# Optimization experiments

Measured on AMD Instinct MI355X. Metric: run time of the kernel, lower is better.

The kernel has to match this reference:

```python
import jax, jax.numpy as jnp
import numpy as np
import math

B, N0, DEG = 32, 1584, 4
E = B * N0 * DEG
FIN, HID, EDIM, ROUTE, HEADS = 32, 64, 8, 16, 4
NEG = 0.2  # leaky_relu negative slope (alpha)
K1 = math.ceil(0.8 * N0)   # 1268 nodes/graph after pool1
K2 = math.ceil(0.8 * K1)   # 1015 after pool2
K3 = math.ceil(0.8 * K2)   # 812 after pool3


def _gatv2(x, src, dst, emask, edge_attr, Wl, bl, Wr, br, We, att, bo, num_nodes):
    # PyG GATv2Conv, concat=False (mean over heads), edge_dim, eval mode (no dropout)
    xl = (x @ Wl + bl).reshape(-1, HEADS, HID)            # source transform  [N,H,C]
    xr = (x @ Wr + br).reshape(-1, HEADS, HID)            # target transform  [N,H,C]
    ee = (edge_attr @ We).reshape(-1, HEADS, HID)         # edge transform    [E,H,C]
    m = jax.nn.leaky_relu(xl[src] + xr[dst] + ee, NEG)    # [E,H,C]
    logits = jnp.einsum('ehc,hc->eh', m, att)             # [E,H]
    logits = jnp.where(emask[:, None], logits, -jnp.inf)
    mx = jax.ops.segment_max(logits, dst, num_segments=num_nodes)
    mx = jnp.where(jnp.isfinite(mx), mx, 0.0)             # nodes w/o in-edges
    ex = jnp.where(emask[:, None], jnp.exp(logits - mx[dst]), 0.0)
    den = jax.ops.segment_sum(ex, dst, num_segments=num_nodes)
    alpha = ex / jnp.maximum(den[dst], 1e-16)             # segment softmax over dst
    out = jax.ops.segment_sum(alpha[:, :, None] * xl[src], dst, num_segments=num_nodes)
    return out.mean(axis=1) + bo                          # concat=False -> head mean


def _topk(x, src, dst, emask, w, n_per, k):
    # PyG TopKPooling(ratio=0.8): score = tanh(x.w/||w||); keep top-k per graph,
    # scale kept features by score; keep edges whose endpoints both survive.
    s = jnp.tanh((x @ w) / jnp.linalg.norm(w))            # [B*n_per]
    _, idx = jax.lax.top_k(s.reshape(B, n_per), k)        # [B,k]
    perm = (idx + jnp.arange(B)[:, None] * n_per).reshape(-1)
    x_new = x[perm] * s[perm][:, None]
    new_id = jnp.full((B * n_per,), -1, jnp.int32).at[perm].set(
        jnp.arange(B * k, dtype=jnp.int32))
    nsrc, ndst = new_id[src], new_id[dst]
    m = emask & (nsrc >= 0) & (ndst >= 0)
    return x_new, jnp.where(m, nsrc, 0), jnp.where(m, ndst, 0), m


def _readout(x, k):
    # global mean pool || global max pool (nodes are grouped per graph, k each)
    xb = x.reshape(B, k, HID)
    return jnp.concatenate([xb.mean(1), xb.max(1)], axis=1)


def _forward(x, edge_attr, edge_index,
             g1_Wl, g1_bl, g1_Wr, g1_br, g1_We, g1_att, g1_b,
             g2_Wl, g2_bl, g2_Wr, g2_br, g2_We, g2_att, g2_b,
             g3_Wl, g3_bl, g3_Wr, g3_br, g3_We, g3_att, g3_b,
             p1_w, p2_w, p3_w,
             fc1_W, fc1_b, fc2_W, fc2_b, fc3_W, fc3_b):
    src, dst = edge_index[0], edge_index[1]
    emask = jnp.ones((E,), bool)
    h = jax.nn.relu(_gatv2(x, src, dst, emask, edge_attr,
                           g1_Wl, g1_bl, g1_Wr, g1_br, g1_We, g1_att, g1_b, B * N0))
    h, src, dst, emask = _topk(h, src, dst, emask, p1_w, N0, K1)
    x1 = _readout(h, K1)
    h = jax.nn.relu(_gatv2(h, src, dst, emask, edge_attr,
                           g2_Wl, g2_bl, g2_Wr, g2_br, g2_We, g2_att, g2_b, B * K1))
    h, src, dst, emask = _topk(h, src, dst, emask, p2_w, K1, K2)
    x2 = _readout(h, K2)
    h = jax.nn.relu(_gatv2(h, src, dst, emask, edge_attr,
                           g3_Wl, g3_bl, g3_Wr, g3_br, g3_We, g3_att, g3_b, B * K2))
    h, src, dst, emask = _topk(h, src, dst, emask, p3_w, K2, K3)
    x3 = _readout(h, K3)
    r = x1 + x2 + x3                                      # [B, 2*HID]
    h = jax.nn.relu(r @ fc1_W + fc1_b)
    h = jax.nn.relu(h @ fc2_W + fc2_b)                    # dropout results unused in source
    return jax.nn.softmax(h @ fc3_W + fc3_b, axis=1)      # [B, ROUTE]


def setup_inputs() -> dict:
    key = jax.random.key(0)
    ks = iter(jax.random.split(key, 64))
    def nrm(shape, scale):
        return jax.random.normal(next(ks), shape, jnp.float32) * scale
    x = nrm((B * N0, FIN), 1.0)
    srcl = jax.random.randint(next(ks), (B, N0 * DEG), 0, N0)
    dstl = jax.random.randint(next(ks), (B, N0 * DEG), 0, N0)
    off = (jnp.arange(B) * N0)[:, None]
    edge_index = jnp.stack([(srcl + off).reshape(-1),
                            (dstl + off).reshape(-1)]).astype(jnp.int32)
    edge_attr = nrm((E, EDIM), 1.0)
    batch = jnp.repeat(jnp.arange(B, dtype=jnp.int32), N0)
    inp = {"x": x, "edge_attr": edge_attr, "edge_index": edge_index, "batch": batch}
    for li, fin in ((1, FIN), (2, HID), (3, HID)):
        g = 1.0 / np.sqrt(fin)
        inp[f"g{li}_Wl"] = nrm((fin, HEADS * HID), g)
        inp[f"g{li}_bl"] = nrm((HEADS * HID,), 0.02)
        inp[f"g{li}_Wr"] = nrm((fin, HEADS * HID), g)
        inp[f"g{li}_br"] = nrm((HEADS * HID,), 0.02)
        inp[f"g{li}_We"] = nrm((EDIM, HEADS * HID), 1.0 / np.sqrt(EDIM))
        inp[f"g{li}_att"] = nrm((HEADS, HID), 1.0 / np.sqrt(HID))
        inp[f"g{li}_b"] = nrm((HID,), 0.02)
    for li in (1, 2, 3):
        inp[f"p{li}_w"] = nrm((HID,), 1.0 / np.sqrt(HID))
    for fin, fout, nm in ((2 * HID, HID, "fc1"), (HID, HID, "fc2"), (HID, ROUTE, "fc3")):
        inp[f"{nm}_W"] = nrm((fin, fout), 1.0 / np.sqrt(fin))
        inp[f"{nm}_b"] = nrm((fout,), 0.02)
    return inp


def reference(x, edge_attr, edge_index, batch,
              g1_Wl, g1_bl, g1_Wr, g1_br, g1_We, g1_att, g1_b,
              g2_Wl, g2_bl, g2_Wr, g2_br, g2_We, g2_att, g2_b,
              g3_Wl, g3_bl, g3_Wr, g3_br, g3_We, g3_att, g3_b,
              p1_w, p2_w, p3_w,
              fc1_W, fc1_b, fc2_W, fc2_b, fc3_W, fc3_b):
    # batch is implicit: nodes are laid out grouped per graph with static sizes
    del batch
    return _forward(x, edge_attr, edge_index,
                    g1_Wl, g1_bl, g1_Wr, g1_br, g1_We, g1_att, g1_b,
                    g2_Wl, g2_bl, g2_Wr, g2_br, g2_We, g2_att, g2_b,
                    g3_Wl, g3_bl, g3_Wr, g3_br, g3_We, g3_att, g3_b,
                    p1_w, p2_w, p3_w,
                    fc1_W, fc1_b, fc2_W, fc2_b, fc3_W, fc3_b)
```

## Files before the change

### kernel.cpp

```cpp
#include <hip/hip_runtime.h>

typedef unsigned short u16;
typedef unsigned int u32;
typedef unsigned long long u64;

#define E_TOT 202752
#define NMAX  50688
#define HEADS 4
#define B_    32
#define MAXDEG 32
#define REMAP_Y 25

#define CDIV(a,b) (((a)+(b)-1)/(b))

__device__ __forceinline__ u32 ford(float f) {
  u32 u = __float_as_uint(f);
  return (u & 0x80000000u) ? ~u : (u | 0x80000000u);
}
__device__ __forceinline__ float ford_inv(u32 u) {
  u32 b = (u & 0x80000000u) ? (u ^ 0x80000000u) : ~u;
  return __uint_as_float(b);
}

template <int CTRL>
__device__ __forceinline__ float dpp_mov(float x) {
  return __int_as_float(__builtin_amdgcn_mov_dpp(__float_as_int(x), CTRL, 0xF, 0xF, false));
}
__device__ __forceinline__ float row16_sum(float v) {
  v += dpp_mov<0x121>(v);
  v += dpp_mov<0x122>(v);
  v += dpp_mov<0x124>(v);
  v += dpp_mov<0x128>(v);
  return v;
}

__device__ __forceinline__ u64 shfl_xor_u64(u64 v, int mask) {
  int lo = __shfl_xor((int)(u32)(v & 0xFFFFFFFFu), mask, 64);
  int hi = __shfl_xor((int)(u32)(v >> 32), mask, 64);
  return ((u64)(u32)hi << 32) | (u32)lo;
}

__global__ void k_edge_init_csr(const int* __restrict__ ei, int* __restrict__ src,
                                int* __restrict__ dst, int* __restrict__ em,
                                int* __restrict__ cnt, int* __restrict__ csr) {
  int e = blockIdx.x * blockDim.x + threadIdx.x;
  if (e >= E_TOT) return;
  int s = ei[e], d = ei[E_TOT + e];
  src[e] = s;
  dst[e] = d;
  em[e] = 1;
  int pos = atomicAdd(&cnt[d], 1);
  if (pos < MAXDEG) csr[d * MAXDEG + pos] = e;
}

template <int FIN>
__global__ void k_transform_t(const float* __restrict__ hin,
                              const float* __restrict__ Wl, const float* __restrict__ bl,
                              const float* __restrict__ Wr, const float* __restrict__ br,
                              float* __restrict__ xl, float* __restrict__ xr) {
  __shared__ float xs[FIN][20];
  int n0 = blockIdx.x * 16, j = threadIdx.x;
  for (int t = j; t < 16 * FIN; t += 256) {
    int nd = t >> (FIN == 32 ? 5 : 6), f = t & (FIN - 1);
    xs[f][nd] = hin[(size_t)(n0 + nd) * FIN + f];
  }
  __syncthreads();
  float al[16], ar[16];
  float blv = bl[j], brv = br[j];
#pragma unroll
  for (int t = 0; t < 16; ++t) { al[t] = blv; ar[t] = brv; }
  for (int i = 0; i < FIN; ++i) {
    float wl = Wl[i * 256 + j], wr = Wr[i * 256 + j];
    float4 x0 = *(const float4*)&xs[i][0];
    float4 x1 = *(const float4*)&xs[i][4];
    float4 x2 = *(const float4*)&xs[i][8];
    float4 x3 = *(const float4*)&xs[i][12];
    al[0]  += x0.x * wl; ar[0]  += x0.x * wr;
    al[1]  += x0.y * wl; ar[1]  += x0.y * wr;
    al[2]  += x0.z * wl; ar[2]  += x0.z * wr;
    al[3]  += x0.w * wl; ar[3]  += x0.w * wr;
    al[4]  += x1.x * wl; ar[4]  += x1.x * wr;
    al[5]  += x1.y * wl; ar[5]  += x1.y * wr;
    al[6]  += x1.z * wl; ar[6]  += x1.z * wr;
    al[7]  += x1.w * wl; ar[7]  += x1.w * wr;
    al[8]  += x2.x * wl; ar[8]  += x2.x * wr;
    al[9]  += x2.y * wl; ar[9]  += x2.y * wr;
    al[10] += x2.z * wl; ar[10] += x2.z * wr;
    al[11] += x2.w * wl; ar[11] += x2.w * wr;
    al[12] += x3.x * wl; ar[12] += x3.x * wr;
    al[13] += x3.y * wl; ar[13] += x3.y * wr;
    al[14] += x3.z * wl; ar[14] += x3.z * wr;
    al[15] += x3.w * wl; ar[15] += x3.w * wr;
  }
#pragma unroll
  for (int t = 0; t < 16; ++t) {
    xl[(size_t)(n0 + t) * 256 + j] = al[t];
    xr[(size_t)(n0 + t) * 256 + j] = ar[t];
  }
}

__global__ void k_gat_fused(const int* __restrict__ srcv, const int* __restrict__ cnt,
                            const int* __restrict__ csr, const float* __restrict__ ea,
                            const float* __restrict__ We, const float* __restrict__ att,
                            const float* __restrict__ xl, const float* __restrict__ xr,
                            const float* __restrict__ bias, const float* __restrict__ pwv,
                            float* __restrict__ out, float* __restrict__ sc,
                            int n_per) {
  int b = blockIdx.x;
  int xcd = b & 7;
  int jj = b >> 3;
  int g = xcd + 8 * (jj >> 6);
  int wv = ((jj & 63) << 2) + (threadIdx.x >> 6);
  int lane = threadIdx.x & 63;
  int cg = lane & 15;
  int cb = (lane >> 4) * 64 + cg * 4;
  int npw = CDIV(n_per, 256);
  int l0 = wv * npw, l1 = min(n_per, l0 + npw);
  if (l0 >= n_per) return;
  int n0 = g * n_per + l0, n1 = g * n_per + l1;
  float4 at4 = *(const float4*)(att + cb);
  float4 w0 = *(const float4*)(We + 0 * 256 + cb);
  float4 w1 = *(const float4*)(We + 1 * 256 + cb);
  float4 w2 = *(const float4*)(We + 2 * 256 + cb);
  float4 w3 = *(const float4*)(We + 3 * 256 + cb);
  float4 w4_ = *(const float4*)(We + 4 * 256 + cb);
  float4 w5 = *(const float4*)(We + 5 * 256 + cb);
  float4 w6 = *(const float4*)(We + 6 * 256 + cb);
  float4 w7 = *(const float4*)(We + 7 * 256 + cb);
  float4 bi4 = *(const float4*)(bias + cg * 4);
  float4 pw4 = *(const float4*)(pwv + cg * 4);
  float wn = pw4.x * pw4.x + pw4.y * pw4.y + pw4.z * pw4.z + pw4.w * pw4.w;
  wn += __shfl_xor(wn, 1, 64); wn += __shfl_xor(wn, 2, 64);
  wn += __shfl_xor(wn, 4, 64); wn += __shfl_xor(wn, 8, 64);
  float isq = 1.f / sqrtf(wn);

  int np1 = min(n0 + 1, n1 - 1);
  int deg_0 = cnt[n0];
  int e0v = (lane < MAXDEG) ? csr[n0 * MAXDEG + lane] : 0;
  int s0v = srcv[e0v];
  float4 xd0 = *(const float4*)(xr + (size_t)n0 * 256 + cb);
  int deg_1 = cnt[np1];
  int e1v = (lane < MAXDEG) ? csr[np1 * MAXDEG + lane] : 0;
  int s1v = srcv[e1v];
  float4 xd1 = *(const float4*)(xr + (size_t)np1 * 256 + cb);
  float4 pxs[4], pa0[4], pa1[4];
#pragma unroll
  for (int j = 0; j < 4; ++j) {
    int ee = __builtin_amdgcn_readlane(e0v, j);
    int ss = __builtin_amdgcn_readlane(s0v, j);
    pxs[j] = *(const float4*)(xl + (size_t)ss * 256 + cb);
    pa0[j] = *(const float4*)(ea + (size_t)ee * 8);
    pa1[j] = *(const float4*)(ea + (size_t)ee * 8 + 4);
  }

  for (int n = n0; n < n1; ++n) {
    int np2 = min(n + 2, n1 - 1);
    int deg_2 = cnt[np2];
    int e2v = (lane < MAXDEG) ? csr[np2 * MAXDEG + lane] : 0;
    int s2v = srcv[e2v];
    float4 xd2 = *(const float4*)(xr + (size_t)np2 * 256 + cb);

    int deg = min(deg_0, MAXDEG);
    float4 xd4 = xd0;
    float m = -INFINITY, l = 0.f;
    float ox = 0.f, oy = 0.f, oz = 0.f, ow = 0.f;

    if (deg > 0) {
      int c0 = deg < 4 ? deg : 4;
      float v[4];
#pragma unroll
      for (int j = 0; j < 4; ++j) {
        if (j < c0) {
          float e0 = pa0[j].x * w0.x + pa0[j].y * w1.x + pa0[j].z * w2.x + pa0[j].w * w3.x
                   + pa1[j].x * w4_.x + pa1[j].y * w5.x + pa1[j].z * w6.x + pa1[j].w * w7.x;
          float e1 = pa0[j].x * w0.y + pa0[j].y * w1.y + pa0[j].z * w2.y + pa0[j].w * w3.y
                   + pa1[j].x * w4_.y + pa1[j].y * w5.y + pa1[j].z * w6.y + pa1[j].w * w7.y;
          float e2 = pa0[j].x * w0.z + pa0[j].y * w1.z + pa0[j].z * w2.z + pa0[j].w * w3.z
                   + pa1[j].x * w4_.z + pa1[j].y * w5.z + pa1[j].z * w6.z + pa1[j].w * w7.z;
          float e3 = pa0[j].x * w0.w + pa0[j].y * w1.w + pa0[j].z * w2.w + pa0[j].w * w3.w
                   + pa1[j].x * w4_.w + pa1[j].y * w5.w + pa1[j].z * w6.w + pa1[j].w * w7.w;
          float m0 = pxs[j].x + xd4.x + e0; m0 = (m0 >= 0.f) ? m0 : 0.2f * m0;
          float m1 = pxs[j].y + xd4.y + e1; m1 = (m1 >= 0.f) ? m1 : 0.2f * m1;
          float m2 = pxs[j].z + xd4.z + e2; m2 = (m2 >= 0.f) ? m2 : 0.2f * m2;
          float m3 = pxs[j].w + xd4.w + e3; m3 = (m3 >= 0.f) ? m3 : 0.2f * m3;
          float d = at4.x * m0 + at4.y * m1 + at4.z * m2 + at4.w * m3;
          v[j] = row16_sum(d);
        } else {
          v[j] = -INFINITY;
        }
      }
      float vm = fmaxf(fmaxf(v[0], v[1]), fmaxf(v[2], v[3]));
      float nm = vm;
      float p0 = __expf(v[0] - nm), p1 = __expf(v[1] - nm);
      float p2 = __expf(v[2] - nm), p3 = __expf(v[3] - nm);
      ox = (p0 * pxs[0].x + p1 * pxs[1].x) + (p2 * pxs[2].x + p3 * pxs[3].x);
      oy = (p0 * pxs[0].y + p1 * pxs[1].y) + (p2 * pxs[2].y + p3 * pxs[3].y);
      oz = (p0 * pxs[0].z + p1 * pxs[1].z) + (p2 * pxs[2].z + p3 * pxs[3].z);
      ow = (p0 * pxs[0].w + p1 * pxs[1].w) + (p2 * pxs[2].w + p3 * pxs[3].w);
      l = (p0 + p1) + (p2 + p3);
      m = nm;
      for (int i0 = 4; i0 < deg; i0 += 4) {
        int c0i = deg - i0; if (c0i > 4) c0i = 4;
        float4 ixs[4], ia0[4], ia1[4];
#pragma unroll
        for (int j = 0; j < 4; ++j) {
          int idx = (j < c0i) ? (i0 + j) : i0;
          int e = __builtin_amdgcn_readlane(e0v, idx);
          int s = __builtin_amdgcn_readlane(s0v, idx);
          ixs[j] = *(const float4*)(xl + (size_t)s * 256 + cb);
          ia0[j] = *(const float4*)(ea + (size_t)e * 8);
          ia1[j] = *(const float4*)(ea + (size_t)e * 8 + 4);
        }
        float vv[4];
#pragma unroll
        for (int j = 0; j < 4; ++j) {
          if (j < c0i) {
            float e0 = ia0[j].x * w0.x + ia0[j].y * w1.x + ia0[j].z * w2.x + ia0[j].w * w3.x
                     + ia1[j].x * w4_.x + ia1[j].y * w5.x + ia1[j].z * w6.x + ia1[j].w * w7.x;
            float e1 = ia0[j].x * w0.y + ia0[j].y * w1.y + ia0[j].z * w2.y + ia0[j].w * w3.y
                     + ia1[j].x * w4_.y + ia1[j].y * w5.y + ia1[j].z * w6.y + ia1[j].w * w7.y;
            float e2 = ia0[j].x * w0.z + ia0[j].y * w1.z + ia0[j].z * w2.z + ia0[j].w * w3.z
                     + ia1[j].x * w4_.z + ia1[j].y * w5.z + ia1[j].z * w6.z + ia1[j].w * w7.z;
            float e3 = ia0[j].x * w0.w + ia0[j].y * w1.w + ia0[j].z * w2.w + ia0[j].w * w3.w
                     + ia1[j].x * w4_.w + ia1[j].y * w5.w + ia1[j].z * w6.w + ia1[j].w * w7.w;
            float m0 = ixs[j].x + xd4.x + e0; m0 = (m0 >= 0.f) ? m0 : 0.2f * m0;
            float m1 = ixs[j].y + xd4.y + e1; m1 = (m1 >= 0.f) ? m1 : 0.2f * m1;
            float m2 = ixs[j].z + xd4.z + e2; m2 = (m2 >= 0.f) ? m2 : 0.2f * m2;
            float m3 = ixs[j].w + xd4.w + e3; m3 = (m3 >= 0.f) ? m3 : 0.2f * m3;
            float d = at4.x * m0 + at4.y * m1 + at4.z * m2 + at4.w * m3;
            vv[j] = row16_sum(d);
          } else {
            vv[j] = -INFINITY;
          }
        }
        float vmi = fmaxf(fmaxf(vv[0], vv[1]), fmaxf(vv[2], vv[3]));
        float nmi = fmaxf(m, vmi);
        float scale = __expf(m - nmi);
        float q0 = __expf(vv[0] - nmi), q1 = __expf(vv[1] - nmi);
        float q2 = __expf(vv[2] - nmi), q3 = __expf(vv[3] - nmi);
        ox = ox * scale + ((q0 * ixs[0].x + q1 * ixs[1].x) + (q2 * ixs[2].x + q3 * ixs[3].x));
        oy = oy * scale + ((q0 * ixs[0].y + q1 * ixs[1].y) + (q2 * ixs[2].y + q3 * ixs[3].y));
        oz = oz * scale + ((q0 * ixs[0].z + q1 * ixs[1].z) + (q2 * ixs[2].z + q3 * ixs[3].z));
        ow = ow * scale + ((q0 * ixs[0].w + q1 * ixs[1].w) + (q2 * ixs[2].w + q3 * ixs[3].w));
        l = l * scale + ((q0 + q1) + (q2 + q3));
        m = nmi;
      }
    }

#pragma unroll
    for (int j = 0; j < 4; ++j) {
      int ee = __builtin_amdgcn_readlane(e1v, j);
      int ss = __builtin_amdgcn_readlane(s1v, j);
      pxs[j] = *(const float4*)(xl + (size_t)ss * 256 + cb);
      pa0[j] = *(const float4*)(ea + (size_t)ee * 8);
      pa1[j] = *(const float4*)(ea + (size_t)ee * 8 + 4);
    }

    float inv = 0.25f / fmaxf(l, 1e-16f);
    float r0 = ox * inv, r1 = oy * inv, r2 = oz * inv, r3 = ow * inv;
    r0 += __shfl_xor(r0, 16, 64); r0 += __shfl_xor(r0, 32, 64);
    r1 += __shfl_xor(r1, 16, 64); r1 += __shfl_xor(r1, 32, 64);
    r2 += __shfl_xor(r2, 16, 64); r2 += __shfl_xor(r2, 32, 64);
    r3 += __shfl_xor(r3, 16, 64); r3 += __shfl_xor(r3, 32, 64);
    float rr0 = fmaxf(r0 + bi4.x, 0.f), rr1 = fmaxf(r1 + bi4.y, 0.f);
    float rr2 = fmaxf(r2 + bi4.z, 0.f), rr3 = fmaxf(r3 + bi4.w, 0.f);
    if (lane < 16) *(float4*)(out + (size_t)n * 64 + cg * 4) = float4{rr0, rr1, rr2, rr3};
    float dot = rr0 * pw4.x + rr1 * pw4.y + rr2 * pw4.z + rr3 * pw4.w;
    dot += __shfl_xor(dot, 1, 64);
    dot += __shfl_xor(dot, 2, 64);
    dot += __shfl_xor(dot, 4, 64);
    dot += __shfl_xor(dot, 8, 64);
    if (lane == 0) sc[n] = tanhf(dot * isq);

    deg_0 = deg_1; e0v = e1v; s0v = s1v; xd0 = xd1;
    deg_1 = deg_2; e1v = e2v; s1v = s2v; xd1 = xd2;
  }
}

__global__ __launch_bounds__(1024) void k_topk(const float* __restrict__ s, int n_per,
                                               int k,
                                               int* __restrict__ perm, int* __restrict__ new_id,
                                               int* __restrict__ cnt) {
  __shared__ u64 kv[2048];
  int b = blockIdx.x, t = threadIdx.x;
  int base = b * n_per;
  for (int i = t; i < n_per; i += 1024) new_id[base + i] = -1;
  for (int i = t; i < k; i += 1024) cnt[b * k + i] = 0;

  u64 e0, e1;
  {
    u32 sk0 = (t < n_per) ? ford(s[base + t]) : 0u;
    int i1 = t + 1024;
    u32 sk1 = (i1 < n_per) ? ford(s[base + i1]) : 0u;
    e0 = ((u64)sk0 << 32) | (u32)(0xFFFFFFFFu - (u32)t);
    e1 = ((u64)sk1 << 32) | (u32)(0xFFFFFFFFu - (u32)i1);
  }

  for (int kk = 2; kk <= 2048; kk <<= 1) {
    int j = kk >> 1;
    if (j == 1024) {
      u64 mx = e0 > e1 ? e0 : e1;
      u64 mn = e0 > e1 ? e1 : e0;
      e0 = mx; e1 = mn;
      j >>= 1;
    }
    for (; j >= 64; j >>= 1) {
      __syncthreads();
      kv[t] = e0; kv[t + 1024] = e1;
      __syncthreads();
      u64 p0 = kv[t ^ j], p1 = kv[(t + 1024) ^ j];
      int i1 = t + 1024;
      bool km0 = (((t  & kk) == 0) == ((t  & j) == 0));
      bool km1 = (((i1 & kk) == 0) == ((i1 & j) == 0));
      e0 = km0 ? (e0 > p0 ? e0 : p0) : (e0 < p0 ? e0 : p0);
      e1 = km1 ? (e1 > p1 ? e1 : p1) : (e1 < p1 ? e1 : p1);
    }
    for (; j >= 1; j >>= 1) {
      u64 p0 = shfl_xor_u64(e0, j);
      u64 p1 = shfl_xor_u64(e1, j);
      int i1 = t + 1024;
      bool km0 = (((t  & kk) == 0) == ((t  & j) == 0));
      bool km1 = (((i1 & kk) == 0) == ((i1 & j) == 0));
      e0 = km0 ? (e0 > p0 ? e0 : p0) : (e0 < p0 ? e0 : p0);
      e1 = km1 ? (e1 > p1 ? e1 : p1) : (e1 < p1 ? e1 : p1);
    }
  }

  if (t < k) {
    int old0 = (int)(0xFFFFFFFFu - (u32)(e0 & 0xFFFFFFFFu));
    perm[b * k + t] = base + old0;
    new_id[base + old0] = b * k + t;
  }
  int r1 = t + 1024;
  if (r1 < k) {
    int old1 = (int)(0xFFFFFFFFu - (u32)(e1 & 0xFFFFFFFFu));
    perm[b * k + r1] = base + old1;
    new_id[base + old1] = b * k + r1;
  }
}

__global__ void k_post(const float* __restrict__ hin, const float* __restrict__ s,
                       const int* __restrict__ perm, float* __restrict__ hout,
                       int k, int gather_rows,
                       float* __restrict__ rsum, u32* __restrict__ rmaxI,
                       int* __restrict__ src, int* __restrict__ dst, int* __restrict__ em,
                       const int* __restrict__ new_id, int* __restrict__ cnt,
                       int* __restrict__ csr, int do_remap) {
  __shared__ float ps[256], pm[256];
  int b = blockIdx.x, yy = blockIdx.y, t = threadIdx.x;
  if (yy < gather_rows) {
    int i = yy * 4 + (t >> 6);
    int c = t & 63;
    bool valid = i < k;
    float v = 0.f;
    if (valid) {
      int g = perm[b * k + i];
      v = hin[(size_t)g * 64 + c] * s[g];
      hout[((size_t)b * k + i) * 64 + c] = v;
    }
    ps[t] = valid ? v : 0.f;
    pm[t] = valid ? v : -INFINITY;
    __syncthreads();
    if (t < 64) {
      float s4 = ps[t] + ps[t + 64] + ps[t + 128] + ps[t + 192];
      float m4 = fmaxf(fmaxf(pm[t], pm[t + 64]), fmaxf(pm[t + 128], pm[t + 192]));
      atomicAdd(&rsum[b * 64 + t], s4);
      atomicMax(&rmaxI[b * 64 + t], ford(m4));
    }
  } else if (do_remap) {
    int e = ((yy - gather_rows) * 32 + b) * 256 + t;
    if (e < E_TOT) {
      int ns = new_id[src[e]], nd = new_id[dst[e]];
      int mm = em[e] && ns >= 0 && nd >= 0;
      src[e] = mm ? ns : 0;
      dst[e] = mm ? nd : 0;
      em[e] = mm;
      if (mm) {
        int pos = atomicAdd(&cnt[nd], 1);
        if (pos < MAXDEG) csr[nd * MAXDEG + pos] = e;
      }
    }
  }
}

__global__ void k_mlp(const char* __restrict__ rblk,
                      const float* __restrict__ W1, const float* __restrict__ b1,
                      const float* __restrict__ W2, const float* __restrict__ b2,
                      const float* __restrict__ W3, const float* __restrict__ b3,
                      float* __restrict__ out) {
  __shared__ float v0[128], v1[64], v2[64], lgts[16];
  int b = blockIdx.x, t = threadIdx.x;
  const float* rs0 = (const float*)rblk;
  const u32*   rm0 = (const u32*)(rblk + 32 * 64 * 4);
  const float* rs1 = (const float*)(rblk + 32 * 128 * 4);
  const u32*   rm1 = (const u32*)(rblk + 32 * 128 * 4 + 32 * 64 * 4);
  const float* rs2 = (const float*)(rblk + 2 * 32 * 128 * 4);
  const u32*   rm2 = (const u32*)(rblk + 2 * 32 * 128 * 4 + 32 * 64 * 4);
  v0[t] = rs0[b * 64 + t] / 1268.f + rs1[b * 64 + t] / 1015.f + rs2[b * 64 + t] / 812.f;
  v0[64 + t] = ford_inv(rm0[b * 64 + t]) + ford_inv(rm1[b * 64 + t]) + ford_inv(rm2[b * 64 + t]);
  __syncthreads();
  float a = b1[t];
  for (int i = 0; i < 128; ++i) a += v0[i] * W1[i * 64 + t];
  v1[t] = fmaxf(a, 0.f);
  __syncthreads();
  a = b2[t];
  for (int i = 0; i < 64; ++i) a += v1[i] * W2[i * 64 + t];
  v2[t] = fmaxf(a, 0.f);
  __syncthreads();
  if (t < 16) {
    a = b3[t];
    for (int i = 0; i < 64; ++i) a += v2[i] * W3[i * 16 + t];
    lgts[t] = a;
  }
  __syncthreads();
  if (t == 0) {
    float m = lgts[0];
    for (int j = 1; j < 16; ++j) m = fmaxf(m, lgts[j]);
    float ex[16], sum = 0.f;
    for (int j = 0; j < 16; ++j) { ex[j] = expf(lgts[j] - m); sum += ex[j]; }
    for (int j = 0; j < 16; ++j) out[b * 16 + j] = ex[j] / sum;
  }
}

extern "C" void kernel_launch(void* const* d_in, const int* in_sizes, int n_in,
                              void* d_out, int out_size, void* d_ws, size_t ws_size,
                              hipStream_t stream) {
  (void)in_sizes; (void)n_in; (void)out_size; (void)ws_size;
  const float* x  = (const float*)d_in[0];
  const float* ea = (const float*)d_in[1];
  const int*   ei = (const int*)d_in[2];

  const float *gWl[3], *gbl[3], *gWr[3], *gbr[3], *gWe[3], *gatt[3], *gb[3], *pw[3];
  for (int l = 0; l < 3; ++l) {
    int p0 = 4 + 7 * l;
    gWl[l]  = (const float*)d_in[p0 + 0];
    gbl[l]  = (const float*)d_in[p0 + 1];
    gWr[l]  = (const float*)d_in[p0 + 2];
    gbr[l]  = (const float*)d_in[p0 + 3];
    gWe[l]  = (const float*)d_in[p0 + 4];
    gatt[l] = (const float*)d_in[p0 + 5];
    gb[l]   = (const float*)d_in[p0 + 6];
    pw[l]   = (const float*)d_in[25 + l];
  }
  const float* fc1W = (const float*)d_in[28];
  const float* fc1b = (const float*)d_in[29];
  const float* fc2W = (const float*)d_in[30];
  const float* fc2b = (const float*)d_in[31];
  const float* fc3W = (const float*)d_in[32];
  const float* fc3b = (const float*)d_in[33];

  char* w = (char*)d_ws;
  size_t off = 0;
  auto alloc = [&](size_t bytes) -> void* {
    void* p = w + off;
    off += (bytes + 255) & ~(size_t)255;
    return p;
  };
  float* hbuf = (float*)alloc((size_t)B_ * 1268 * 64 * 4);
  float* xl   = (float*)alloc((size_t)NMAX * 256 * 4);
  float* xr   = (float*)alloc((size_t)NMAX * 256 * 4);
  float* nacc = (float*)alloc((size_t)NMAX * 64 * 4);
  int*   cnt  = (int*)alloc((size_t)NMAX * 4);
  char*  rblk = (char*)alloc(3 * 32 * 128 * 4);
  int*   csr  = (int*)alloc((size_t)NMAX * MAXDEG * 4);
  float* sbuf = (float*)alloc((size_t)NMAX * 4);
  int* src    = (int*)alloc((size_t)E_TOT * 4);
  int* dst    = (int*)alloc((size_t)E_TOT * 4);
  int* em     = (int*)alloc((size_t)E_TOT * 4);
  int* new_id = (int*)alloc((size_t)NMAX * 4);
  int* perm   = (int*)alloc((size_t)32 * 1268 * 4);

  size_t zbytes = (size_t)NMAX * 4 + 3 * 32 * 128 * 4 + (size_t)NMAX * MAXDEG * 4;
  hipMemsetAsync(cnt, 0, zbytes, stream);
  k_edge_init_csr<<<CDIV(E_TOT, 256), 256, 0, stream>>>(ei, src, dst, em, cnt, csr);

  const int Ns[3]    = {50688, 40576, 32480};
  const int npers[3] = {1584, 1268, 1015};
  const int ks[3]    = {1268, 1015, 812};
  const int GAT_BLOCKS = 2048;

  for (int l = 0; l < 3; ++l) {
    int N = Ns[l];
    const float* hin = (l == 0) ? x : hbuf;
    float* rsum = (float*)(rblk + l * 32 * 128 * 4);
    u32* rmaxI  = (u32*)(rblk + l * 32 * 128 * 4 + 32 * 64 * 4);
    if (l == 0)
      k_transform_t<32><<<N / 16, 256, 0, stream>>>(hin, gWl[l], gbl[l], gWr[l], gbr[l], xl, xr);
    else
      k_transform_t<64><<<N / 16, 256, 0, stream>>>(hin, gWl[l], gbl[l], gWr[l], gbr[l], xl, xr);
    k_gat_fused<<<GAT_BLOCKS, 256, 0, stream>>>(src, cnt, csr, ea, gWe[l], gatt[l],
                                                xl, xr, gb[l], pw[l], nacc, sbuf, npers[l]);
    k_topk<<<32, 1024, 0, stream>>>(sbuf, npers[l], ks[l], perm, new_id, cnt);
    int grows = CDIV(ks[l], 4);
    dim3 pgrid(32, grows + (l < 2 ? REMAP_Y : 0));
    k_post<<<pgrid, 256, 0, stream>>>(nacc, sbuf, perm, hbuf, ks[l], grows, rsum, rmaxI,
                                      src, dst, em, new_id, cnt, csr, (l < 2) ? 1 : 0);
  }
  k_mlp<<<32, 64, 0, stream>>>(rblk, fc1W, fc1b, fc2W, fc2b, fc3W, fc3b, (float*)d_out);
}
```

Before: 521.9 us.

## Fuse edge CSR build into layer-1 transform and shorten GAT prefetch depth

```diff
diff --git a/kernel.cpp b/kernel.cpp
--- a/kernel.cpp
+++ b/kernel.cpp
@@ -10,6 +10,8 @@
 #define B_    32
 #define MAXDEG 32
 #define REMAP_Y 25
+#define TRE_TBLK 3168
+#define TRE_EBLK 792
 
 #define CDIV(a,b) (((a)+(b)-1)/(b))
 
@@ -40,17 +42,64 @@
   return ((u64)(u32)hi << 32) | (u32)lo;
 }
 
-__global__ void k_edge_init_csr(const int* __restrict__ ei, int* __restrict__ src,
-                                int* __restrict__ dst, int* __restrict__ em,
-                                int* __restrict__ cnt, int* __restrict__ csr) {
-  int e = blockIdx.x * blockDim.x + threadIdx.x;
-  if (e >= E_TOT) return;
-  int s = ei[e], d = ei[E_TOT + e];
-  src[e] = s;
-  dst[e] = d;
-  em[e] = 1;
-  int pos = atomicAdd(&cnt[d], 1);
-  if (pos < MAXDEG) csr[d * MAXDEG + pos] = e;
+__global__ void k_tre(const float* __restrict__ hin,
+                      const float* __restrict__ Wl, const float* __restrict__ bl,
+                      const float* __restrict__ Wr, const float* __restrict__ br,
+                      float* __restrict__ xl, float* __restrict__ xr,
+                      const int* __restrict__ ei, int* __restrict__ src,
+                      int* __restrict__ dst, int* __restrict__ em,
+                      int* __restrict__ cnt, int* __restrict__ csr) {
+  __shared__ float xs[32][20];
+  int j = threadIdx.x;
+  if (blockIdx.x >= TRE_TBLK) {
+    int e = (blockIdx.x - TRE_TBLK) * 256 + j;
+    if (e >= E_TOT) return;
+    int s = ei[e], d = ei[E_TOT + e];
+    src[e] = s;
+    dst[e] = d;
+    em[e] = 1;
+    int pos = atomicAdd(&cnt[d], 1);
+    if (pos < MAXDEG) csr[d * MAXDEG + pos] = e;
+    return;
+  }
+  int n0 = blockIdx.x * 16;
+  for (int t = j; t < 16 * 32; t += 256) {
+    int nd = t >> 5, f = t & 31;
+    xs[f][nd] = hin[(size_t)(n0 + nd) * 32 + f];
+  }
+  __syncthreads();
+  float al[16], ar[16];
+  float blv = bl[j], brv = br[j];
+#pragma unroll
+  for (int t = 0; t < 16; ++t) { al[t] = blv; ar[t] = brv; }
+  for (int i = 0; i < 32; ++i) {
+    float wl = Wl[i * 256 + j], wr = Wr[i * 256 + j];
+    float4 x0 = *(const float4*)&xs[i][0];
+    float4 x1 = *(const float4*)&xs[i][4];
+    float4 x2 = *(const float4*)&xs[i][8];
+    float4 x3 = *(const float4*)&xs[i][12];
+    al[0]  += x0.x * wl; ar[0]  += x0.x * wr;
+    al[1]  += x0.y * wl; ar[1]  += x0.y * wr;
+    al[2]  += x0.z * wl; ar[2]  += x0.z * wr;
+    al[3]  += x0.w * wl; ar[3]  += x0.w * wr;
+    al[4]  += x1.x * wl; ar[4]  += x1.x * wr;
+    al[5]  += x1.y * wl; ar[5]  += x1.y * wr;
+    al[6]  += x1.z * wl; ar[6]  += x1.z * wr;
+    al[7]  += x1.w * wl; ar[7]  += x1.w * wr;
+    al[8]  += x2.x * wl; ar[8]  += x2.x * wr;
+    al[9]  += x2.y * wl; ar[9]  += x2.y * wr;
+    al[10] += x2.z * wl; ar[10] += x2.z * wr;
+    al[11] += x2.w * wl; ar[11] += x2.w * wr;
+    al[12] += x3.x * wl; ar[12] += x3.x * wr;
+    al[13] += x3.y * wl; ar[13] += x3.y * wr;
+    al[14] += x3.z * wl; ar[14] += x3.z * wr;
+    al[15] += x3.w * wl; ar[15] += x3.w * wr;
+  }
+#pragma unroll
+  for (int t = 0; t < 16; ++t) {
+    xl[(size_t)(n0 + t) * 256 + j] = al[t];
+    xr[(size_t)(n0 + t) * 256 + j] = ar[t];
+  }
 }
 
 template <int FIN>
@@ -99,7 +148,8 @@
   }
 }
 
-__global__ void k_gat_fused(const int* __restrict__ srcv, const int* __restrict__ cnt,
+__global__ __launch_bounds__(256, 4) void k_gat_fused(
+                            const int* __restrict__ srcv, const int* __restrict__ cnt,
                             const int* __restrict__ csr, const float* __restrict__ ea,
                             const float* __restrict__ We, const float* __restrict__ att,
                             const float* __restrict__ xl, const float* __restrict__ xr,
@@ -134,34 +184,31 @@
   wn += __shfl_xor(wn, 4, 64); wn += __shfl_xor(wn, 8, 64);
   float isq = 1.f / sqrtf(wn);
 
-  int np1 = min(n0 + 1, n1 - 1);
-  int deg_0 = cnt[n0];
-  int e0v = (lane < MAXDEG) ? csr[n0 * MAXDEG + lane] : 0;
-  int s0v = srcv[e0v];
-  float4 xd0 = *(const float4*)(xr + (size_t)n0 * 256 + cb);
-  int deg_1 = cnt[np1];
-  int e1v = (lane < MAXDEG) ? csr[np1 * MAXDEG + lane] : 0;
-  int s1v = srcv[e1v];
-  float4 xd1 = *(const float4*)(xr + (size_t)np1 * 256 + cb);
+  int degc = cnt[n0];
+  int e_c = (lane < MAXDEG) ? csr[n0 * MAXDEG + lane] : 0;
+  int s_c = srcv[e_c];
+  float4 xdc = *(const float4*)(xr + (size_t)n0 * 256 + cb);
   float4 pxs[4], pa0[4], pa1[4];
 #pragma unroll
   for (int j = 0; j < 4; ++j) {
-    int ee = __builtin_amdgcn_readlane(e0v, j);
-    int ss = __builtin_amdgcn_readlane(s0v, j);
+    int ee = __builtin_amdgcn_readlane(e_c, j);
+    int ss = __builtin_amdgcn_readlane(s_c, j);
     pxs[j] = *(const float4*)(xl + (size_t)ss * 256 + cb);
     pa0[j] = *(const float4*)(ea + (size_t)ee * 8);
     pa1[j] = *(const float4*)(ea + (size_t)ee * 8 + 4);
   }
 
   for (int n = n0; n < n1; ++n) {
-    int np2 = min(n + 2, n1 - 1);
-    int deg_2 = cnt[np2];
-    int e2v = (lane < MAXDEG) ? csr[np2 * MAXDEG + lane] : 0;
-    int s2v = srcv[e2v];
-    float4 xd2 = *(const float4*)(xr + (size_t)np2 * 256 + cb);
-
-    int deg = min(deg_0, MAXDEG);
-    float4 xd4 = xd0;
+    int degn = 0, e_n = 0, s_n = 0;
+    float4 xdn = xdc;
+    if (n + 1 < n1) {
+      degn = cnt[n + 1];
+      e_n = (lane < MAXDEG) ? csr[(n + 1) * MAXDEG + lane] : 0;
+      s_n = srcv[e_n];
+      xdn = *(const float4*)(xr + (size_t)(n + 1) * 256 + cb);
+    }
+    int deg = min(degc, MAXDEG);
+    float4 xd4 = xdc;
     float m = -INFINITY, l = 0.f;
     float ox = 0.f, oy = 0.f, oz = 0.f, ow = 0.f;
 
@@ -205,8 +252,8 @@
 #pragma unroll
         for (int j = 0; j < 4; ++j) {
           int idx = (j < c0i) ? (i0 + j) : i0;
-          int e = __builtin_amdgcn_readlane(e0v, idx);
-          int s = __builtin_amdgcn_readlane(s0v, idx);
+          int e = __builtin_amdgcn_readlane(e_c, idx);
+          int s = __builtin_amdgcn_readlane(s_c, idx);
           ixs[j] = *(const float4*)(xl + (size_t)s * 256 + cb);
           ia0[j] = *(const float4*)(ea + (size_t)e * 8);
           ia1[j] = *(const float4*)(ea + (size_t)e * 8 + 4);
@@ -249,8 +296,8 @@
 
 #pragma unroll
     for (int j = 0; j < 4; ++j) {
-      int ee = __builtin_amdgcn_readlane(e1v, j);
-      int ss = __builtin_amdgcn_readlane(s1v, j);
+      int ee = __builtin_amdgcn_readlane(e_n, j);
+      int ss = __builtin_amdgcn_readlane(s_n, j);
       pxs[j] = *(const float4*)(xl + (size_t)ss * 256 + cb);
       pa0[j] = *(const float4*)(ea + (size_t)ee * 8);
       pa1[j] = *(const float4*)(ea + (size_t)ee * 8 + 4);
@@ -271,9 +318,7 @@
     dot += __shfl_xor(dot, 4, 64);
     dot += __shfl_xor(dot, 8, 64);
     if (lane == 0) sc[n] = tanhf(dot * isq);
-
-    deg_0 = deg_1; e0v = e1v; s0v = s1v; xd0 = xd1;
-    deg_1 = deg_2; e1v = e2v; s1v = s2v; xd1 = xd2;
+    degc = degn; e_c = e_n; s_c = s_n; xdc = xdn;
   }
 }
 
@@ -472,7 +517,6 @@
 
   size_t zbytes = (size_t)NMAX * 4 + 3 * 32 * 128 * 4 + (size_t)NMAX * MAXDEG * 4;
   hipMemsetAsync(cnt, 0, zbytes, stream);
-  k_edge_init_csr<<<CDIV(E_TOT, 256), 256, 0, stream>>>(ei, src, dst, em, cnt, csr);
 
   const int Ns[3]    = {50688, 40576, 32480};
   const int npers[3] = {1584, 1268, 1015};
@@ -485,7 +529,8 @@
     float* rsum = (float*)(rblk + l * 32 * 128 * 4);
     u32* rmaxI  = (u32*)(rblk + l * 32 * 128 * 4 + 32 * 64 * 4);
     if (l == 0)
-      k_transform_t<32><<<N / 16, 256, 0, stream>>>(hin, gWl[l], gbl[l], gWr[l], gbr[l], xl, xr);
+      k_tre<<<TRE_TBLK + TRE_EBLK, 256, 0, stream>>>(hin, gWl[l], gbl[l], gWr[l], gbr[l],
+                                                     xl, xr, ei, src, dst, em, cnt, csr);
     else
       k_transform_t<64><<<N / 16, 256, 0, stream>>>(hin, gWl[l], gbl[l], gWr[l], gbr[l], xl, xr);
     k_gat_fused<<<GAT_BLOCKS, 256, 0, stream>>>(src, cnt, csr, ea, gWe[l], gatt[l],
```

Result: faster. 470.9 us (-9.8%).
